# Kernel optimization log

Hardware: AMD Instinct MI355X
Metric: run time of the kernel (lower is better)

The kernel has to match this reference:

```python
import jax, jax.numpy as jnp
import numpy as np

D = 256       # d_model
HEADS = 8     # n_heads
PTS = 4       # n_points
FF = 1024     # dim_feedforward
HD = D // HEADS
B, Q = 8, 900
HH, WW = 100, 100


def setup_inputs() -> dict:
    key = jax.random.key(0)
    ks = iter(jax.random.split(key, 40))
    p = lambda shape: jax.random.normal(next(ks), shape, dtype=jnp.float32) * 0.02
    inp = {
        "tgt": jax.random.normal(next(ks), (B, Q, D), dtype=jnp.float32),
        "memory": jax.random.normal(next(ks), (B, HH * WW, D), dtype=jnp.float32),
        "H": HH,
        "W": WW,
        # self-attention (nn.MultiheadAttention) params
        "in_proj_w": p((3 * D, D)), "in_proj_b": p((3 * D,)),
        "out_proj_w": p((D, D)), "out_proj_b": p((D,)),
        # layer norms
        "norm1_s": jnp.ones((D,)), "norm1_b": jnp.zeros((D,)),
        "norm2_s": jnp.ones((D,)), "norm2_b": jnp.zeros((D,)),
        "norm3_s": jnp.ones((D,)), "norm3_b": jnp.zeros((D,)),
        # deformable cross-attention params
        "vproj_w": p((D, D)), "vproj_b": p((D,)),
        "offs_w": p((HEADS * PTS * 2, D)), "offs_b": p((HEADS * PTS * 2,)),
        "attw_w": p((HEADS * PTS, D)), "attw_b": p((HEADS * PTS,)),
        "ref_w": p((2, D)), "ref_b": p((2,)),
        "cout_w": p((D, D)), "cout_b": p((D,)),
        # FFN params
        "ffn_w1": p((FF, D)), "ffn_b1": p((FF,)),
        "ffn_w2": p((D, FF)), "ffn_b2": p((D,)),
    }
    return inp


def _layer_norm(x, s, b):
    m = jnp.mean(x, -1, keepdims=True)
    v = jnp.mean((x - m) ** 2, -1, keepdims=True)
    return (x - m) * jax.lax.rsqrt(v + 1e-5) * s + b


def _mha(x, wi, bi, wo, bo):
    b, q, _ = x.shape
    qkv = x @ wi.T + bi
    qh, kh, vh = jnp.split(qkv, 3, axis=-1)
    qh = qh.reshape(b, q, HEADS, HD).transpose(0, 2, 1, 3)
    kh = kh.reshape(b, q, HEADS, HD).transpose(0, 2, 1, 3)
    vh = vh.reshape(b, q, HEADS, HD).transpose(0, 2, 1, 3)
    att = jax.nn.softmax(jnp.einsum('bhqd,bhkd->bhqk', qh, kh) / np.float32(np.sqrt(HD)), axis=-1)
    o = jnp.einsum('bhqk,bhkd->bhqd', att, vh).transpose(0, 2, 1, 3).reshape(b, q, D)
    return o @ wo.T + bo


def _deform_attn(q, mem, H, W, vproj_w, vproj_b, offs_w, offs_b, attw_w, attw_b,
                 ref_w, ref_b, cout_w, cout_b):
    b, nq, _ = q.shape
    # per-query normalized reference points (x, y) in [0,1]
    ref = jax.nn.sigmoid(q @ ref_w.T + ref_b)                         # [B,Q,2]
    offs = (q @ offs_w.T + offs_b).reshape(b, nq, HEADS, PTS, 2)      # [B,Q,h,p,2]
    attw = jax.nn.softmax((q @ attw_w.T + attw_b).reshape(b, nq, HEADS, PTS), axis=-1)
    val = (mem @ vproj_w.T + vproj_b).reshape(b, H * W, HEADS, HD).transpose(0, 2, 1, 3)  # [B,h,HW,hd]
    wh = jnp.array([W, H], dtype=q.dtype)
    loc = ref[:, :, None, None, :] + offs / wh                        # normalized sampling loc
    x = loc[..., 0] * W - 0.5                                         # pixel coords (align_corners=False)
    y = loc[..., 1] * H - 0.5
    x0 = jnp.floor(x); y0 = jnp.floor(y)
    lx = x - x0; ly = y - y0
    x0i = x0.astype(jnp.int32); y0i = y0.astype(jnp.int32)

    def gather(xi, yi):
        valid = ((xi >= 0) & (xi < W) & (yi >= 0) & (yi < H)).astype(q.dtype)
        idx = jnp.clip(yi, 0, H - 1) * W + jnp.clip(xi, 0, W - 1)     # [B,Q,h,p]
        idxt = idx.transpose(0, 2, 1, 3).reshape(b, HEADS, nq * PTS, 1)
        g = jnp.take_along_axis(val, idxt, axis=2)                    # [B,h,Q*p,hd]
        g = g.reshape(b, HEADS, nq, PTS, HD).transpose(0, 2, 1, 3, 4)  # [B,Q,h,p,hd]
        return g * valid[..., None]

    samp = (gather(x0i, y0i) * ((1 - lx) * (1 - ly))[..., None]
            + gather(x0i + 1, y0i) * (lx * (1 - ly))[..., None]
            + gather(x0i, y0i + 1) * ((1 - lx) * ly)[..., None]
            + gather(x0i + 1, y0i + 1) * (lx * ly)[..., None])        # [B,Q,h,p,hd]
    out = jnp.sum(samp * attw[..., None], axis=3).reshape(b, nq, D)
    return out @ cout_w.T + cout_b


def reference(tgt, memory, H, W, in_proj_w, in_proj_b, out_proj_w, out_proj_b,
              norm1_s, norm1_b, norm2_s, norm2_b, norm3_s, norm3_b,
              vproj_w, vproj_b, offs_w, offs_b, attw_w, attw_b, ref_w, ref_b,
              cout_w, cout_b, ffn_w1, ffn_b1, ffn_w2, ffn_b2):
    t2 = _mha(tgt, in_proj_w, in_proj_b, out_proj_w, out_proj_b)
    t = _layer_norm(tgt + t2, norm1_s, norm1_b)
    t2 = _deform_attn(t, memory, H, W, vproj_w, vproj_b, offs_w, offs_b,
                      attw_w, attw_b, ref_w, ref_b, cout_w, cout_b)
    t = _layer_norm(t + t2, norm2_s, norm2_b)
    f = jnp.maximum(t @ ffn_w1.T + ffn_b1, 0) @ ffn_w2.T + ffn_b2
    return _layer_norm(t + f, norm3_s, norm3_b)
```

## Files before the change

### kernel.cpp

```cpp
#include <hip/hip_runtime.h>
#include <hip/hip_bf16.h>

typedef __hip_bfloat16 bf16;
typedef __attribute__((ext_vector_type(8))) short short8;
typedef __attribute__((ext_vector_type(4))) float f32x4;

#define BB 8
#define QQ 900
#define DD 256
#define NH 8
#define HD 32
#define NPTS 4
#define FFD 1024
#define HH 100
#define WW2 100
#define HWTOT 10000

#define QT 64
#define KTC 128
#define NCHUNK ((QQ + KTC - 1) / KTC)
#define QB 4

__device__ inline float tofloat(float x) { return x; }
__device__ inline float tofloat(bf16 x) { return __bfloat162float(x); }
__device__ inline float bf2f(unsigned short u) {
    return __uint_as_float(((unsigned int)u) << 16);
}
__device__ inline void storev(bf16* p, float v) { *p = __float2bfloat16(v); }
__device__ inline void storev(float* p, float v) { *p = v; }

__global__ void pack_kernel(const float* __restrict__ in_proj_w, const float* __restrict__ out_proj_w,
                            const float* __restrict__ cout_w, const float* __restrict__ ffn_w1,
                            const float* __restrict__ ffn_w2, const float* __restrict__ vproj_w,
                            const float* __restrict__ offs_w, const float* __restrict__ attw_w,
                            const float* __restrict__ ref_w, const float* __restrict__ offs_b,
                            const float* __restrict__ attw_b, const float* __restrict__ ref_b,
                            const float* __restrict__ tgt, bf16* __restrict__ wpk,
                            bf16* __restrict__ tgtb, float* __restrict__ dbias) {
    const int idx = blockIdx.x * 256 + threadIdx.x;
    const int TOT = 950272 + 1843200 + 128;
    if (idx >= TOT) return;
    if (idx < 196608) {
        wpk[idx] = __float2bfloat16(in_proj_w[idx]);
    } else if (idx < 262144) {
        wpk[idx] = __float2bfloat16(out_proj_w[idx - 196608]);
    } else if (idx < 327680) {
        wpk[idx] = __float2bfloat16(cout_w[idx - 262144]);
    } else if (idx < 589824) {
        wpk[idx] = __float2bfloat16(ffn_w1[idx - 327680]);
    } else if (idx < 851968) {
        wpk[idx] = __float2bfloat16(ffn_w2[idx - 589824]);
    } else if (idx < 917504) {
        wpk[idx] = __float2bfloat16(vproj_w[idx - 851968]);
    } else if (idx < 950272) {
        const int j = idx - 917504;
        const int r = j >> 8, c = j & 255;
        float v = 0.f;
        if (r < 64) v = offs_w[r * 256 + c];
        else if (r < 96) v = attw_w[(r - 64) * 256 + c];
        else if (r < 98) v = ref_w[(r - 96) * 256 + c];
        wpk[idx] = __float2bfloat16(v);
    } else if (idx < 950272 + 1843200) {
        const int j = idx - 950272;
        tgtb[j] = __float2bfloat16(tgt[j]);
    } else {
        const int j = idx - (950272 + 1843200);
        float v = 0.f;
        if (j < 64) v = offs_b[j];
        else if (j < 96) v = attw_b[j - 64];
        else if (j < 98) v = ref_b[j - 96];
        dbias[j] = v;
    }
}

template <int ACT, typename OT>
__global__ __launch_bounds__(256) void gemm_mfma_kernel(const bf16* __restrict__ A,
                                                        const bf16* __restrict__ W,
                                                        const float* __restrict__ bias,
                                                        OT* __restrict__ C, int M, int N, int K) {
    __shared__ unsigned short As[64][56];
    __shared__ unsigned short Bs[64][56];
    const int bm = blockIdx.y * 64, bn = blockIdx.x * 64;
    const int tid = threadIdx.x;
    const int lane = tid & 63, wave = tid >> 6;
    const int sr = tid >> 2, sc = (tid & 3) * 8;
    f32x4 acc[4] = {{0.f, 0.f, 0.f, 0.f}, {0.f, 0.f, 0.f, 0.f},
                    {0.f, 0.f, 0.f, 0.f}, {0.f, 0.f, 0.f, 0.f}};
    const uint4 zero4 = {0u, 0u, 0u, 0u};
    for (int k0 = 0; k0 < K; k0 += 32) {
        __syncthreads();
        {
            const int arow = bm + sr;
            uint4 a4 = (arow < M) ? *(const uint4*)(A + (size_t)arow * K + k0 + sc) : zero4;
            *(uint4*)&As[sr][sc] = a4;
            const int wrow = bn + sr;
            uint4 b4 = (wrow < N) ? *(const uint4*)(W + (size_t)wrow * K + k0 + sc) : zero4;
            *(uint4*)&Bs[sr][sc] = b4;
        }
        __syncthreads();
        const short8 af = *(const short8*)&As[wave * 16 + (lane & 15)][(lane >> 4) * 8];
#pragma unroll
        for (int ct = 0; ct < 4; ++ct) {
            const short8 bf = *(const short8*)&Bs[ct * 16 + (lane & 15)][(lane >> 4) * 8];
            acc[ct] = __builtin_amdgcn_mfma_f32_16x16x32_bf16(af, bf, acc[ct], 0, 0, 0);
        }
    }
#pragma unroll
    for (int ct = 0; ct < 4; ++ct) {
        const int col = bn + ct * 16 + (lane & 15);
        const float bv = bias[col];
#pragma unroll
        for (int r = 0; r < 4; ++r) {
            const int row = bm + wave * 16 + (lane >> 4) * 4 + r;
            if (row < M) {
                float v = acc[ct][r] + bv;
                if (ACT == 1) v = fmaxf(v, 0.f);
                storev(&C[(size_t)row * N + col], v);
            }
        }
    }
}

__global__ __launch_bounds__(256) void mha_mfma_kernel(const bf16* __restrict__ qkv,
                                                       bf16* __restrict__ o) {
    const int qt = blockIdx.x, h = blockIdx.y, b = blockIdx.z;
    const int tid = threadIdx.x;
    const int lane = tid & 63, wave = tid >> 6;
    const int l15 = lane & 15, g = lane >> 4;
    __shared__ unsigned short Kls[KTC][40];
    __shared__ bf16 Vt[HD][136];
    __shared__ bf16 Pls[4][16][136];
    const size_t base = (size_t)b * QQ * 768;
    const int q0 = qt * QT;

    short8 qa = {0, 0, 0, 0, 0, 0, 0, 0};
    {
        const int qg = q0 + wave * 16 + l15;
        if (qg < QQ)
            qa = *(const short8*)(qkv + base + (size_t)qg * 768 + h * HD + g * 8);
    }
    f32x4 accO[2] = {{0.f, 0.f, 0.f, 0.f}, {0.f, 0.f, 0.f, 0.f}};
    float m_run[4], l_run[4];
#pragma unroll
    for (int r = 0; r < 4; ++r) {
        m_run[r] = -1e30f;
        l_run[r] = 0.f;
    }
    const float scale = 0.17677669529663687f;
    const uint4 zero4 = {0u, 0u, 0u, 0u};

    for (int c = 0; c < NCHUNK; ++c) {
        const int k0 = c * KTC;
        __syncthreads();
        {
            const int part = tid & 3, kr = tid >> 2;
#pragma unroll
            for (int pass = 0; pass < 2; ++pass) {
                const int krr = kr + pass * 64;
                const int kg = k0 + krr;
                uint4 kv = (kg < QQ)
                    ? *(const uint4*)(qkv + base + (size_t)kg * 768 + DD + h * HD + part * 8)
                    : zero4;
                *(uint4*)&Kls[krr][part * 8] = kv;
            }
        }
        {
            const int kr = tid >> 1, ch0 = (tid & 1) * 16;
            const int kg = k0 + kr;
            uint4 v0 = zero4, v1 = zero4;
            if (kg < QQ) {
                const bf16* pv = qkv + base + (size_t)kg * 768 + 2 * DD + h * HD + ch0;
                v0 = *(const uint4*)pv;
                v1 = *(const uint4*)(pv + 8);
            }
            const unsigned short* u0 = (const unsigned short*)&v0;
            const unsigned short* u1 = (const unsigned short*)&v1;
#pragma unroll
            for (int j = 0; j < 8; ++j) {
                ((unsigned short*)&Vt[ch0 + j][kr])[0] = u0[j];
                ((unsigned short*)&Vt[ch0 + 8 + j][kr])[0] = u1[j];
            }
        }
        __syncthreads();

        f32x4 s[8];
#pragma unroll
        for (int t = 0; t < 8; ++t) {
            const short8 kb = *(const short8*)&Kls[t * 16 + l15][g * 8];
            const f32x4 z = {0.f, 0.f, 0.f, 0.f};
            s[t] = __builtin_amdgcn_mfma_f32_16x16x32_bf16(qa, kb, z, 0, 0, 0);
        }
        float mx[4] = {-1e30f, -1e30f, -1e30f, -1e30f};
#pragma unroll
        for (int t = 0; t < 8; ++t) {
            const bool cv = (k0 + t * 16 + l15) < QQ;
#pragma unroll
            for (int r = 0; r < 4; ++r) {
                const float v = cv ? s[t][r] * scale : -1e30f;
                s[t][r] = v;
                mx[r] = fmaxf(mx[r], v);
            }
        }
#pragma unroll
        for (int r = 0; r < 4; ++r) {
            mx[r] = fmaxf(mx[r], __shfl_xor(mx[r], 1));
            mx[r] = fmaxf(mx[r], __shfl_xor(mx[r], 2));
            mx[r] = fmaxf(mx[r], __shfl_xor(mx[r], 4));
            mx[r] = fmaxf(mx[r], __shfl_xor(mx[r], 8));
        }
        float alpha[4], rs[4];
#pragma unroll
        for (int r = 0; r < 4; ++r) {
            const float mn = fmaxf(m_run[r], mx[r]);
            alpha[r] = __expf(m_run[r] - mn);
            m_run[r] = mn;
            rs[r] = 0.f;
        }
#pragma unroll
        for (int t = 0; t < 8; ++t) {
#pragma unroll
            for (int r = 0; r < 4; ++r) {
                const float p = __expf(s[t][r] - m_run[r]);
                rs[r] += p;
                Pls[wave][g * 4 + r][t * 16 + l15] = __float2bfloat16(p);
            }
        }
#pragma unroll
        for (int r = 0; r < 4; ++r) {
            rs[r] += __shfl_xor(rs[r], 1);
            rs[r] += __shfl_xor(rs[r], 2);
            rs[r] += __shfl_xor(rs[r], 4);
            rs[r] += __shfl_xor(rs[r], 8);
            l_run[r] = l_run[r] * alpha[r] + rs[r];
        }
#pragma unroll
        for (int t2 = 0; t2 < 2; ++t2)
#pragma unroll
            for (int r = 0; r < 4; ++r) accO[t2][r] *= alpha[r];
#pragma unroll
        for (int s4 = 0; s4 < 4; ++s4) {
            const short8 pa = *(const short8*)&Pls[wave][l15][s4 * 32 + g * 8];
#pragma unroll
            for (int t2 = 0; t2 < 2; ++t2) {
                const short8 vb = *(const short8*)&Vt[t2 * 16 + l15][s4 * 32 + g * 8];
                accO[t2] = __builtin_amdgcn_mfma_f32_16x16x32_bf16(pa, vb, accO[t2], 0, 0, 0);
            }
        }
    }
#pragma unroll
    for (int r = 0; r < 4; ++r) {
        const int row = q0 + wave * 16 + g * 4 + r;
        if (row < QQ) {
            const float inv = 1.f / l_run[r];
#pragma unroll
            for (int t2 = 0; t2 < 2; ++t2) {
                storev(&o[((size_t)b * QQ + row) * DD + h * HD + t2 * 16 + l15],
                       accO[t2][r] * inv);
            }
        }
    }
}

template <typename TR, typename TO>
__global__ void add_ln_kernel(const TR* __restrict__ resid, const bf16* __restrict__ y,
                              const float* __restrict__ g, const float* __restrict__ bta,
                              TO* __restrict__ out) {
    const int row = blockIdx.x;
    const int tid = threadIdx.x;
    __shared__ float red[256];
    const size_t idx = (size_t)row * DD + tid;
    float v = tofloat(resid[idx]) + tofloat(y[idx]);
    red[tid] = v;
    __syncthreads();
    for (int s = 128; s > 0; s >>= 1) {
        if (tid < s) red[tid] += red[tid + s];
        __syncthreads();
    }
    const float mean = red[0] * (1.f / DD);
    __syncthreads();
    const float d = v - mean;
    red[tid] = d * d;
    __syncthreads();
    for (int s = 128; s > 0; s >>= 1) {
        if (tid < s) red[tid] += red[tid + s];
        __syncthreads();
    }
    const float rstd = rsqrtf(red[0] * (1.f / DD) + 1e-5f);
    storev(&out[idx], d * rstd * g[tid] + bta[tid]);
}

__global__ __launch_bounds__(256) void deform_gather_kernel(
    const float* __restrict__ dots, const float* __restrict__ mem,
    bf16* __restrict__ G, float* __restrict__ wsumg) {
    const int qt = blockIdx.x, b = blockIdx.y;
    const int tid = threadIdx.x;
    const int q0 = qt * QB;
    __shared__ int sidx[QB][32][4];
    __shared__ float swt[QB][32][4];

    if (tid < 128) {
        const int q = tid >> 5, hp = tid & 31;
        const float* dr = dots + ((size_t)b * QQ + q0 + q) * 128;
        const float ox = dr[hp * 2], oy = dr[hp * 2 + 1];
        float ad = dr[64 + hp];
        const float rx = dr[96], ry = dr[97];
        float mx = ad;
        mx = fmaxf(mx, __shfl_xor(mx, 1));
        mx = fmaxf(mx, __shfl_xor(mx, 2));
        float e = __expf(ad - mx);
        float sm = e;
        sm += __shfl_xor(sm, 1);
        sm += __shfl_xor(sm, 2);
        const float a = e / sm;
        const float refx = 1.f / (1.f + __expf(-rx));
        const float refy = 1.f / (1.f + __expf(-ry));
        const float x = (refx + ox * (1.f / WW2)) * WW2 - 0.5f;
        const float y = (refy + oy * (1.f / HH)) * HH - 0.5f;
        const float x0f = floorf(x), y0f = floorf(y);
        const float lx = x - x0f, ly = y - y0f;
        const int x0 = (int)x0f, y0 = (int)y0f;
        const float cw[4] = {(1 - lx) * (1 - ly), lx * (1 - ly), (1 - lx) * ly, lx * ly};
        const int cx[4] = {x0, x0 + 1, x0, x0 + 1};
        const int cy[4] = {y0, y0, y0 + 1, y0 + 1};
        float cs = 0.f;
#pragma unroll
        for (int cc = 0; cc < 4; ++cc) {
            const bool valid = cx[cc] >= 0 && cx[cc] < WW2 && cy[cc] >= 0 && cy[cc] < HH;
            const int xi = min(max(cx[cc], 0), WW2 - 1);
            const int yi = min(max(cy[cc], 0), HH - 1);
            sidx[q][hp][cc] = yi * WW2 + xi;
            const float w = valid ? a * cw[cc] : 0.f;
            swt[q][hp][cc] = w;
            cs += w;
        }
        cs += __shfl_xor(cs, 1);
        cs += __shfl_xor(cs, 2);
        if ((hp & 3) == 0) wsumg[((size_t)b * QQ + q0 + q) * NH + (hp >> 2)] = cs;
    }
    __syncthreads();

    {
        const int q = tid >> 6, cbase = (tid & 63) * 4;
        const float* mb = mem + (size_t)b * HWTOT * DD;
        bf16* gq = G + ((size_t)(b * QQ + q0 + q) * NH) * DD + cbase;
#pragma unroll
        for (int h = 0; h < NH; ++h) {
            float4 acc = {0.f, 0.f, 0.f, 0.f};
#pragma unroll
            for (int p = 0; p < NPTS; ++p) {
                const int hp = h * NPTS + p;
                const int4 ix = *(const int4*)sidx[q][hp];
                const float4 wt = *(const float4*)swt[q][hp];
                const float4 v0 = *(const float4*)(mb + (size_t)ix.x * DD + cbase);
                const float4 v1 = *(const float4*)(mb + (size_t)ix.y * DD + cbase);
                const float4 v2 = *(const float4*)(mb + (size_t)ix.z * DD + cbase);
                const float4 v3 = *(const float4*)(mb + (size_t)ix.w * DD + cbase);
                acc.x += wt.x * v0.x + wt.y * v1.x + wt.z * v2.x + wt.w * v3.x;
                acc.y += wt.x * v0.y + wt.y * v1.y + wt.z * v2.y + wt.w * v3.y;
                acc.z += wt.x * v0.z + wt.y * v1.z + wt.z * v2.z + wt.w * v3.z;
                acc.w += wt.x * v0.w + wt.y * v1.w + wt.z * v2.w + wt.w * v3.w;
            }
            bf16 out4[4] = {__float2bfloat16(acc.x), __float2bfloat16(acc.y),
                            __float2bfloat16(acc.z), __float2bfloat16(acc.w)};
            *(uint2*)(gq + (size_t)h * DD) = *(const uint2*)out4;
        }
    }
}

__global__ __launch_bounds__(256) void gemm_vproj_kernel(
    const bf16* __restrict__ G, const bf16* __restrict__ Wv,
    const float* __restrict__ vb, const float* __restrict__ wsumg,
    bf16* __restrict__ samp, int M) {
    __shared__ unsigned short As[64][40];
    __shared__ unsigned short Bs[32][40];
    const int h = blockIdx.x, bm = blockIdx.y * 64;
    const int tid = threadIdx.x;
    const int lane = tid & 63, wave = tid >> 6;
    const int l15 = lane & 15, g = lane >> 4;
    const int sr = tid >> 2, sc = (tid & 3) * 8;
    f32x4 acc[2] = {{0.f, 0.f, 0.f, 0.f}, {0.f, 0.f, 0.f, 0.f}};
    const uint4 zero4 = {0u, 0u, 0u, 0u};
    for (int k0 = 0; k0 < DD; k0 += 32) {
        __syncthreads();
        {
            const int arow = bm + sr;
            uint4 a4 = (arow < M)
                ? *(const uint4*)(G + ((size_t)arow * NH + h) * DD + k0 + sc)
                : zero4;
            *(uint4*)&As[sr][sc] = a4;
            if (sr < 32) {
                uint4 b4 = *(const uint4*)(Wv + (size_t)(h * 32 + sr) * DD + k0 + sc);
                *(uint4*)&Bs[sr][sc] = b4;
            }
        }
        __syncthreads();
        const short8 af = *(const short8*)&As[wave * 16 + l15][g * 8];
#pragma unroll
        for (int ct = 0; ct < 2; ++ct) {
            const short8 bf = *(const short8*)&Bs[ct * 16 + l15][g * 8];
            acc[ct] = __builtin_amdgcn_mfma_f32_16x16x32_bf16(af, bf, acc[ct], 0, 0, 0);
        }
    }
#pragma unroll
    for (int ct = 0; ct < 2; ++ct) {
        const int col = h * 32 + ct * 16 + l15;
        const float bv = vb[col];
#pragma unroll
        for (int r = 0; r < 4; ++r) {
            const int row = bm + wave * 16 + g * 4 + r;
            if (row < M) {
                const float v = acc[ct][r] + bv * wsumg[(size_t)row * NH + h];
                storev(&samp[(size_t)row * DD + col], v);
            }
        }
    }
}

extern "C" void kernel_launch(void* const* d_in, const int* in_sizes, int n_in,
                              void* d_out, int out_size, void* d_ws, size_t ws_size,
                              hipStream_t stream) {
    const float* tgt = (const float*)d_in[0];
    const float* memory = (const float*)d_in[1];
    const float* in_proj_w = (const float*)d_in[4];
    const float* in_proj_b = (const float*)d_in[5];
    const float* out_proj_w = (const float*)d_in[6];
    const float* out_proj_b = (const float*)d_in[7];
    const float* norm1_s = (const float*)d_in[8];
    const float* norm1_b = (const float*)d_in[9];
    const float* norm2_s = (const float*)d_in[10];
    const float* norm2_b = (const float*)d_in[11];
    const float* norm3_s = (const float*)d_in[12];
    const float* norm3_b = (const float*)d_in[13];
    const float* vproj_w = (const float*)d_in[14];
    const float* vproj_b = (const float*)d_in[15];
    const float* offs_w = (const float*)d_in[16];
    const float* offs_b = (const float*)d_in[17];
    const float* attw_w = (const float*)d_in[18];
    const float* attw_b = (const float*)d_in[19];
    const float* ref_w = (const float*)d_in[20];
    const float* ref_b = (const float*)d_in[21];
    const float* cout_w = (const float*)d_in[22];
    const float* cout_b = (const float*)d_in[23];
    const float* ffn_w1 = (const float*)d_in[24];
    const float* ffn_b1 = (const float*)d_in[25];
    const float* ffn_w2 = (const float*)d_in[26];
    const float* ffn_b2 = (const float*)d_in[27];

    const int M = BB * QQ;
    bf16* ws = (bf16*)d_ws;
    size_t off = 0;
    bf16* qkv = ws + off;  off += (size_t)M * 768;
    bf16* o = ws + off;    off += (size_t)M * DD;
    bf16* t1 = ws + off;   off += (size_t)M * DD;
    bf16* tmp = ws + off;  off += (size_t)M * DD;
    bf16* ffh = ws + off;  off += (size_t)M * FFD;
    bf16* tgtb = ws + off; off += (size_t)M * DD;
    bf16* wpk = ws + off;  off += 950272;
    float* dbias = (float*)(ws + off); off += 256;
    float* wsumg = (float*)(ws + off); off += (size_t)M * NH * 2;
    bf16* Gws = ws + off;  off += (size_t)M * NH * DD;
    bf16* samp = o;
    bf16* t2n = qkv;
    float* dots = (float*)ffh;

    bf16* w_in = wpk;
    bf16* w_out = wpk + 196608;
    bf16* w_cout = wpk + 262144;
    bf16* w_ffn1 = wpk + 327680;
    bf16* w_ffn2 = wpk + 589824;
    bf16* w_vproj = wpk + 851968;
    bf16* w_dots = wpk + 917504;

    const int MT = (M + 63) / 64;

    pack_kernel<<<(950272 + 1843200 + 128 + 255) / 256, 256, 0, stream>>>(
        in_proj_w, out_proj_w, cout_w, ffn_w1, ffn_w2, vproj_w, offs_w, attw_w, ref_w,
        offs_b, attw_b, ref_b, tgt, wpk, tgtb, dbias);
    gemm_mfma_kernel<0, bf16><<<dim3(12, MT), 256, 0, stream>>>(tgtb, w_in, in_proj_b, qkv,
                                                                M, 768, DD);
    mha_mfma_kernel<<<dim3((QQ + QT - 1) / QT, NH, BB), 256, 0, stream>>>(qkv, o);
    gemm_mfma_kernel<0, bf16><<<dim3(4, MT), 256, 0, stream>>>(o, w_out, out_proj_b, tmp,
                                                               M, DD, DD);
    add_ln_kernel<float, bf16><<<M, 256, 0, stream>>>(tgt, tmp, norm1_s, norm1_b, t1);
    gemm_mfma_kernel<0, float><<<dim3(2, MT), 256, 0, stream>>>(t1, w_dots, dbias, dots,
                                                                M, 128, DD);
    deform_gather_kernel<<<dim3(QQ / QB, BB), 256, 0, stream>>>(dots, memory, Gws, wsumg);
    gemm_vproj_kernel<<<dim3(NH, MT), 256, 0, stream>>>(Gws, w_vproj, vproj_b, wsumg,
                                                        samp, M);
    gemm_mfma_kernel<0, bf16><<<dim3(4, MT), 256, 0, stream>>>(samp, w_cout, cout_b, tmp,
                                                               M, DD, DD);
    add_ln_kernel<bf16, bf16><<<M, 256, 0, stream>>>(t1, tmp, norm2_s, norm2_b, t2n);
    gemm_mfma_kernel<1, bf16><<<dim3(16, MT), 256, 0, stream>>>(t2n, w_ffn1, ffn_b1, ffh,
                                                                M, FFD, DD);
    gemm_mfma_kernel<0, bf16><<<dim3(4, MT), 256, 0, stream>>>(ffh, w_ffn2, ffn_b2, tmp,
                                                               M, DD, FFD);
    add_ln_kernel<bf16, float><<<M, 256, 0, stream>>>(t2n, tmp, norm3_s, norm3_b,
                                                      (float*)d_out);
}
```

Before: 369.3 us.

## Enlarge GEMM tiles with direct global-to-LDS loads and wave-shuffle layernorm

Rewrites the generic MFMA GEMM to use 128-row tiles with a configurable 64 or 128 column width, a 2x2 wave grid and a 4xN accumulator array per wave. This raises MFMA work per LDS fragment load. Operand tiles are now loaded with global_load_lds straight into shared memory instead of staging through registers. The layernorm reduction switches from a shared-memory tree to wave shuffles plus a four-entry cross-wave sum. Larger tiles mean fewer blocks for M=7200, which may leave CUs underused on the narrow-N GEMMs, and the unpadded LDS layout may cause bank conflicts.

Measured after the change: 370.1 us. No clear change (+0.2%).

```diff
diff --git a/kernel.cpp b/kernel.cpp
--- a/kernel.cpp
+++ b/kernel.cpp
@@ -28,6 +28,14 @@
 }
 __device__ inline void storev(bf16* p, float v) { *p = __float2bfloat16(v); }
 __device__ inline void storev(float* p, float v) { *p = v; }
+
+typedef __attribute__((address_space(1))) const unsigned int gas_u32;
+typedef __attribute__((address_space(3))) unsigned int las_u32;
+__device__ inline void gload_lds16(const bf16* g, bf16* l) {
+    __builtin_amdgcn_global_load_lds(
+        (gas_u32*)(unsigned long long)(const void*)g,
+        (las_u32*)(unsigned int)(unsigned long long)(const void*)l, 16, 0, 0);
+}
 
 __global__ void pack_kernel(const float* __restrict__ in_proj_w, const float* __restrict__ out_proj_w,
                             const float* __restrict__ cout_w, const float* __restrict__ ffn_w1,
@@ -73,49 +81,69 @@
     }
 }
 
-template <int ACT, typename OT>
+template <int BN, int ACT, typename OT>
 __global__ __launch_bounds__(256) void gemm_mfma_kernel(const bf16* __restrict__ A,
                                                         const bf16* __restrict__ W,
                                                         const float* __restrict__ bias,
                                                         OT* __restrict__ C, int M, int N, int K) {
-    __shared__ unsigned short As[64][56];
-    __shared__ unsigned short Bs[64][56];
-    const int bm = blockIdx.y * 64, bn = blockIdx.x * 64;
+    constexpr int WC = BN / 2;
+    constexpr int NACC = WC / 16;
+    __shared__ bf16 As[128 * 32];
+    __shared__ bf16 Bs[BN * 32];
+    const int bm = blockIdx.y * 128, bn = blockIdx.x * BN;
     const int tid = threadIdx.x;
     const int lane = tid & 63, wave = tid >> 6;
-    const int sr = tid >> 2, sc = (tid & 3) * 8;
-    f32x4 acc[4] = {{0.f, 0.f, 0.f, 0.f}, {0.f, 0.f, 0.f, 0.f},
-                    {0.f, 0.f, 0.f, 0.f}, {0.f, 0.f, 0.f, 0.f}};
-    const uint4 zero4 = {0u, 0u, 0u, 0u};
+    const int l15 = lane & 15, g = lane >> 4;
+    const int wr = wave >> 1, wc = wave & 1;
+    const int lrow = lane >> 2, lcol = (lane & 3) * 8;
+    const f32x4 zf = {0.f, 0.f, 0.f, 0.f};
+    f32x4 acc[4][NACC];
+#pragma unroll
+    for (int mi = 0; mi < 4; ++mi)
+#pragma unroll
+        for (int ni = 0; ni < NACC; ++ni) acc[mi][ni] = zf;
+
     for (int k0 = 0; k0 < K; k0 += 32) {
         __syncthreads();
-        {
-            const int arow = bm + sr;
-            uint4 a4 = (arow < M) ? *(const uint4*)(A + (size_t)arow * K + k0 + sc) : zero4;
-            *(uint4*)&As[sr][sc] = a4;
-            const int wrow = bn + sr;
-            uint4 b4 = (wrow < N) ? *(const uint4*)(W + (size_t)wrow * K + k0 + sc) : zero4;
-            *(uint4*)&Bs[sr][sc] = b4;
+#pragma unroll
+        for (int i = 0; i < 2; ++i) {
+            const int chunk = wave * 2 + i;
+            const int arow = min(bm + chunk * 16 + lrow, M - 1);
+            gload_lds16(A + (size_t)arow * K + k0 + lcol, &As[chunk * 512]);
+        }
+#pragma unroll
+        for (int i = 0; i < BN / 64; ++i) {
+            const int chunk = wave * (BN / 64) + i;
+            gload_lds16(W + (size_t)(bn + chunk * 16 + lrow) * K + k0 + lcol, &Bs[chunk * 512]);
         }
         __syncthreads();
-        const short8 af = *(const short8*)&As[wave * 16 + (lane & 15)][(lane >> 4) * 8];
-#pragma unroll
-        for (int ct = 0; ct < 4; ++ct) {
-            const short8 bf = *(const short8*)&Bs[ct * 16 + (lane & 15)][(lane >> 4) * 8];
-            acc[ct] = __builtin_amdgcn_mfma_f32_16x16x32_bf16(af, bf, acc[ct], 0, 0, 0);
-        }
-    }
-#pragma unroll
-    for (int ct = 0; ct < 4; ++ct) {
-        const int col = bn + ct * 16 + (lane & 15);
+        short8 af[4];
+#pragma unroll
+        for (int mi = 0; mi < 4; ++mi)
+            af[mi] = *(const short8*)&As[(wr * 64 + mi * 16 + l15) * 32 + g * 8];
+#pragma unroll
+        for (int ni = 0; ni < NACC; ++ni) {
+            const short8 bfv = *(const short8*)&Bs[(wc * WC + ni * 16 + l15) * 32 + g * 8];
+#pragma unroll
+            for (int mi = 0; mi < 4; ++mi)
+                acc[mi][ni] =
+                    __builtin_amdgcn_mfma_f32_16x16x32_bf16(af[mi], bfv, acc[mi][ni], 0, 0, 0);
+        }
+    }
+#pragma unroll
+    for (int ni = 0; ni < NACC; ++ni) {
+        const int col = bn + wc * WC + ni * 16 + l15;
         const float bv = bias[col];
 #pragma unroll
-        for (int r = 0; r < 4; ++r) {
-            const int row = bm + wave * 16 + (lane >> 4) * 4 + r;
-            if (row < M) {
-                float v = acc[ct][r] + bv;
-                if (ACT == 1) v = fmaxf(v, 0.f);
-                storev(&C[(size_t)row * N + col], v);
+        for (int mi = 0; mi < 4; ++mi) {
+#pragma unroll
+            for (int r = 0; r < 4; ++r) {
+                const int row = bm + wr * 64 + mi * 16 + g * 4 + r;
+                if (row < M) {
+                    float v = acc[mi][ni][r] + bv;
+                    if (ACT == 1) v = fmaxf(v, 0.f);
+                    storev(&C[(size_t)row * N + col], v);
+                }
             }
         }
     }
@@ -267,25 +295,24 @@
                               TO* __restrict__ out) {
     const int row = blockIdx.x;
     const int tid = threadIdx.x;
-    __shared__ float red[256];
+    const int lane = tid & 63, wave = tid >> 6;
+    __shared__ float red[4];
     const size_t idx = (size_t)row * DD + tid;
     float v = tofloat(resid[idx]) + tofloat(y[idx]);
-    red[tid] = v;
+    float s = v;
+    s += __shfl_xor(s, 1);  s += __shfl_xor(s, 2);  s += __shfl_xor(s, 4);
+    s += __shfl_xor(s, 8);  s += __shfl_xor(s, 16); s += __shfl_xor(s, 32);
+    if (lane == 0) red[wave] = s;
     __syncthreads();
-    for (int s = 128; s > 0; s >>= 1) {
-        if (tid < s) red[tid] += red[tid + s];
-        __syncthreads();
-    }
-    const float mean = red[0] * (1.f / DD);
+    const float mean = (red[0] + red[1] + red[2] + red[3]) * (1.f / DD);
+    const float d = v - mean;
+    float q = d * d;
+    q += __shfl_xor(q, 1);  q += __shfl_xor(q, 2);  q += __shfl_xor(q, 4);
+    q += __shfl_xor(q, 8);  q += __shfl_xor(q, 16); q += __shfl_xor(q, 32);
     __syncthreads();
-    const float d = v - mean;
-    red[tid] = d * d;
+    if (lane == 0) red[wave] = q;
     __syncthreads();
-    for (int s = 128; s > 0; s >>= 1) {
-        if (tid < s) red[tid] += red[tid + s];
-        __syncthreads();
-    }
-    const float rstd = rsqrtf(red[0] * (1.f / DD) + 1e-5f);
+    const float rstd = rsqrtf((red[0] + red[1] + red[2] + red[3]) * (1.f / DD) + 1e-5f);
     storev(&out[idx], d * rstd * g[tid] + bta[tid]);
 }
 
@@ -472,28 +499,29 @@
     bf16* w_dots = wpk + 917504;
 
     const int MT = (M + 63) / 64;
+    const int MT2 = (M + 127) / 128;
 
     pack_kernel<<<(950272 + 1843200 + 128 + 255) / 256, 256, 0, stream>>>(
         in_proj_w, out_proj_w, cout_w, ffn_w1, ffn_w2, vproj_w, offs_w, attw_w, ref_w,
         offs_b, attw_b, ref_b, tgt, wpk, tgtb, dbias);
-    gemm_mfma_kernel<0, bf16><<<dim3(12, MT), 256, 0, stream>>>(tgtb, w_in, in_proj_b, qkv,
-                                                                M, 768, DD);
+    gemm_mfma_kernel<128, 0, bf16><<<dim3(6, MT2), 256, 0, stream>>>(tgtb, w_in, in_proj_b,
+                                                                     qkv, M, 768, DD);
     mha_mfma_kernel<<<dim3((QQ + QT - 1) / QT, NH, BB), 256, 0, stream>>>(qkv, o);
-    gemm_mfma_kernel<0, bf16><<<dim3(4, MT), 256, 0, stream>>>(o, w_out, out_proj_b, tmp,
-                                                               M, DD, DD);
+    gemm_mfma_kernel<64, 0, bf16><<<dim3(4, MT2), 256, 0, stream>>>(o, w_out, out_proj_b,
+                                                                    tmp, M, DD, DD);
     add_ln_kernel<float, bf16><<<M, 256, 0, stream>>>(tgt, tmp, norm1_s, norm1_b, t1);
-    gemm_mfma_kernel<0, float><<<dim3(2, MT), 256, 0, stream>>>(t1, w_dots, dbias, dots,
-                                                                M, 128, DD);
+    gemm_mfma_kernel<64, 0, float><<<dim3(2, MT2), 256, 0, stream>>>(t1, w_dots, dbias,
+                                                                     dots, M, 128, DD);
     deform_gather_kernel<<<dim3(QQ / QB, BB), 256, 0, stream>>>(dots, memory, Gws, wsumg);
     gemm_vproj_kernel<<<dim3(NH, MT), 256, 0, stream>>>(Gws, w_vproj, vproj_b, wsumg,
                                                         samp, M);
-    gemm_mfma_kernel<0, bf16><<<dim3(4, MT), 256, 0, stream>>>(samp, w_cout, cout_b, tmp,
-                                                               M, DD, DD);
+    gemm_mfma_kernel<64, 0, bf16><<<dim3(4, MT2), 256, 0, stream>>>(samp, w_cout, cout_b,
+                                                                    tmp, M, DD, DD);
     add_ln_kernel<bf16, bf16><<<M, 256, 0, stream>>>(t1, tmp, norm2_s, norm2_b, t2n);
-    gemm_mfma_kernel<1, bf16><<<dim3(16, MT), 256, 0, stream>>>(t2n, w_ffn1, ffn_b1, ffh,
-                                                                M, FFD, DD);
-    gemm_mfma_kernel<0, bf16><<<dim3(4, MT), 256, 0, stream>>>(ffh, w_ffn2, ffn_b2, tmp,
-                                                               M, DD, FFD);
+    gemm_mfma_kernel<128, 1, bf16><<<dim3(8, MT2), 256, 0, stream>>>(t2n, w_ffn1, ffn_b1,
+                                                                     ffh, M, FFD, DD);
+    gemm_mfma_kernel<64, 0, bf16><<<dim3(4, MT2), 256, 0, stream>>>(ffh, w_ffn2, ffn_b2,
+                                                                    tmp, M, DD, FFD);
     add_ln_kernel<bf16, float><<<M, 256, 0, stream>>>(t2n, tmp, norm3_s, norm3_b,
                                                       (float*)d_out);
 }
```
